# Kernel tuning notes

Measured on AMD Instinct MI355X. Metric: run time of the kernel, lower is better.

## Reference

```python
import jax, jax.numpy as jnp
import numpy as np

POOL = 7              # roi_size (output bins per side)
SAMPLING_RATIO = 2    # bilinear samples per bin side
POOLED_DIM = 5        # CEM_FILTER(245) // (7*7)
SPATIAL_SCALE = 0.0625  # 1/16 feature stride


def setup_inputs() -> dict:
    key = jax.random.key(0)
    k1, k2, k3 = jax.random.split(key, 3)
    B, C, H, W = 8, 245, 100, 100
    N = 512
    IMG = 1600.0
    x = jax.random.normal(k1, (B, C, H, W), dtype=jnp.float32)
    xy = jax.random.uniform(k2, (B, N, 2), minval=0.0, maxval=IMG - 256.0)
    wh = jax.random.uniform(k3, (B, N, 2), minval=16.0, maxval=256.0)
    boxes = jnp.concatenate([xy, xy + wh], axis=-1)  # (x1,y1,x2,y2) in image coords
    return {"x": x, "boxes": boxes}


def reference(x, boxes):
    """Position-sensitive RoIAlign (torchvision ps_roi_align semantics).
    x: [B, C=POOLED_DIM*POOL*POOL, H, W]; boxes: [B, N, 4] in image coords.
    Returns [B*N, POOLED_DIM, POOL, POOL]."""
    B, C, H, W = x.shape
    Bb, N, _ = boxes.shape
    R = Bb * N
    g, P, D, s = SAMPLING_RATIO, POOL, POOLED_DIM, SPATIAL_SCALE

    batch_idx = jnp.repeat(jnp.arange(Bb, dtype=jnp.int32), N)  # convert_to_roi_format ids
    rois = boxes.reshape(R, 4)

    # aligned roi coords on the feature map (half-pixel offset)
    start_w = rois[:, 0] * s - 0.5
    start_h = rois[:, 1] * s - 0.5
    end_w = rois[:, 2] * s - 0.5
    end_h = rois[:, 3] * s - 0.5
    bin_h = (end_h - start_h) / P
    bin_w = (end_w - start_w) / P

    p = jnp.arange(P, dtype=jnp.float32)
    i = jnp.arange(g, dtype=jnp.float32)
    # sample coordinates, shape [R, P, g]
    ys = start_h[:, None, None] + p[None, :, None] * bin_h[:, None, None] \
         + (i[None, None, :] + 0.5) * bin_h[:, None, None] / g
    xs = start_w[:, None, None] + p[None, :, None] * bin_w[:, None, None] \
         + (i[None, None, :] + 0.5) * bin_w[:, None, None] / g

    # zero outside [-1, H] / [-1, W] (torchvision bilinear_interpolate)
    vy = ((ys >= -1.0) & (ys <= H)).astype(x.dtype)  # [R,P,g]
    vx = ((xs >= -1.0) & (xs <= W)).astype(x.dtype)

    yc = jnp.clip(ys, 0.0, H - 1.0)
    xc = jnp.clip(xs, 0.0, W - 1.0)
    yl = jnp.floor(yc).astype(jnp.int32)
    xl = jnp.floor(xc).astype(jnp.int32)
    yh = jnp.minimum(yl + 1, H - 1)
    xh = jnp.minimum(xl + 1, W - 1)
    ly = yc - yl.astype(x.dtype); hy = 1.0 - ly
    lx = xc - xl.astype(x.dtype); hx = 1.0 - lx

    # position-sensitive input channel: c_in = (d*P + ph)*P + pw, shape [D,P,P]
    c_in = ((jnp.arange(D)[:, None, None] * P + jnp.arange(P)[None, :, None]) * P
            + jnp.arange(P)[None, None, :]).astype(jnp.int32)

    # broadcast to [R, D, P(h), P(w), g(h), g(w)]
    b = batch_idx[:, None, None, None, None, None]
    c = c_in[None, :, :, :, None, None]
    gy = lambda a: a[:, None, :, None, :, None]  # y-axis arrays [R,P,g]
    gx = lambda a: a[:, None, None, :, None, :]  # x-axis arrays [R,P,g]

    v11 = x[b, c, gy(yl), gx(xl)]
    v12 = x[b, c, gy(yl), gx(xh)]
    v21 = x[b, c, gy(yh), gx(xl)]
    v22 = x[b, c, gy(yh), gx(xh)]
    val = (gy(hy) * gx(hx) * v11 + gy(hy) * gx(lx) * v12
           + gy(ly) * gx(hx) * v21 + gy(ly) * gx(lx) * v22)
    val = val * (gy(vy) * gx(vx))
    out = val.sum(axis=(4, 5)) / (g * g)  # average over sampling grid -> [R, D, P, P]
    return out
```

## Files before the change

### kernel.cpp

```cpp
#include <hip/hip_runtime.h>

#define POOL 7
#define SCALE 0.0625f
#define HW 10000
#define NROI 512
#define NCH 245

typedef const __attribute__((address_space(1))) void* gas_ptr;
typedef __attribute__((address_space(3))) void* las_ptr;

__global__ __launch_bounds__(512) void psroi_kernel(
    const float* __restrict__ x, const float* __restrict__ boxes,
    float* __restrict__ ws, int H, int W)
{
    __shared__ float plane[HW + 4];

    int p = blockIdx.x;
    int b = p / NCH;
    int c = p - b * NCH;
    int ph = (c / POOL) % POOL;
    int pw = c % POOL;

    int n = threadIdx.x;
    int r = b * NROI + n;

    float4 bx = *(const float4*)(boxes + (size_t)r * 4);

    const float4* __restrict__ src4 = (const float4*)(x + (size_t)p * HW);
    int lane = threadIdx.x & 63;
    int wave = threadIdx.x >> 6;
    #pragma unroll
    for (int i = 0; i < 5; ++i) {
        int chunk_base = i * 512 + wave * 64;
        int chunk = chunk_base + lane;
        if (chunk < HW / 4) {
            __builtin_amdgcn_global_load_lds(
                (gas_ptr)(src4 + chunk),
                (las_ptr)((char*)plane + (size_t)chunk_base * 16),
                16, 0, 0);
        }
    }
    if (threadIdx.x < 4) plane[HW + threadIdx.x] = 0.f;

    float sw = bx.x * SCALE - 0.5f;
    float sh = bx.y * SCALE - 0.5f;
    float ew = bx.z * SCALE - 0.5f;
    float eh = bx.w * SCALE - 0.5f;
    float bin_h = (eh - sh) / (float)POOL;
    float bin_w = (ew - sw) / (float)POOL;
    float fy0 = sh + (float)ph * bin_h;
    float fx0 = sw + (float)pw * bin_w;

    int   rowa[2];
    int   rstep[2];
    float wyh[2], wyl[2];
    #pragma unroll
    for (int iy = 0; iy < 2; ++iy) {
        float y  = fy0 + ((float)iy + 0.5f) * bin_h * 0.5f;
        float vy = (y >= -1.0f && y <= (float)H) ? 1.0f : 0.0f;
        float yc = fminf(fmaxf(y, 0.0f), (float)(H - 1));
        int   yl = (int)floorf(yc);
        float ly = yc - (float)yl;
        wyl[iy] = ly * vy;
        wyh[iy] = (1.0f - ly) * vy;
        rowa[iy]  = yl * W;
        rstep[iy] = (yl < H - 1) ? W : 0;
    }
    int   colx[2];
    float wxh[2], wxl[2];
    #pragma unroll
    for (int ix = 0; ix < 2; ++ix) {
        float xf = fx0 + ((float)ix + 0.5f) * bin_w * 0.5f;
        float vx = (xf >= -1.0f && xf <= (float)W) ? 1.0f : 0.0f;
        float xc = fminf(fmaxf(xf, 0.0f), (float)(W - 1));
        int   xl = (int)floorf(xc);
        float lx = xc - (float)xl;
        wxl[ix] = lx * vx;
        wxh[ix] = (1.0f - lx) * vx;
        colx[ix] = xl;
    }

    __syncthreads();

    float sum = 0.f;
    #pragma unroll
    for (int iy = 0; iy < 2; ++iy) {
        #pragma unroll
        for (int ix = 0; ix < 2; ++ix) {
            int a0 = rowa[iy] + colx[ix];
            int a1 = a0 + rstep[iy];
            float v11 = plane[a0];
            float v12 = plane[a0 + 1];
            float v21 = plane[a1];
            float v22 = plane[a1 + 1];
            float top = wxh[ix] * v11 + wxl[ix] * v12;
            float bot = wxh[ix] * v21 + wxl[ix] * v22;
            sum = fmaf(wyh[iy], top, sum);
            sum = fmaf(wyl[iy], bot, sum);
        }
    }
    ws[(size_t)p * NROI + n] = sum * 0.25f;
}

#define TILE 32
__global__ __launch_bounds__(256) void transpose_kernel(
    const float* __restrict__ ws, float* __restrict__ out)
{
    __shared__ float tile[TILE][TILE + 1];
    int b  = blockIdx.z;
    int c0 = blockIdx.y * TILE;
    int n0 = blockIdx.x * TILE;
    const float* in = ws + (size_t)b * NCH * NROI;
    float* ob = out + (size_t)b * NROI * NCH;
    int tx = threadIdx.x;
    int ty = threadIdx.y;

    #pragma unroll
    for (int k = 0; k < 4; ++k) {
        int cc = c0 + ty + k * 8;
        if (cc < NCH) tile[ty + k * 8][tx] = in[(size_t)cc * NROI + n0 + tx];
    }
    __syncthreads();
    #pragma unroll
    for (int k = 0; k < 4; ++k) {
        int nn = n0 + ty + k * 8;
        int cc = c0 + tx;
        if (cc < NCH) ob[(size_t)nn * NCH + cc] = tile[tx][ty + k * 8];
    }
}

extern "C" void kernel_launch(void* const* d_in, const int* in_sizes, int n_in,
                              void* d_out, int out_size, void* d_ws, size_t ws_size,
                              hipStream_t stream) {
    const float* x     = (const float*)d_in[0];
    const float* boxes = (const float*)d_in[1];
    float* out = (float*)d_out;
    float* ws  = (float*)d_ws;

    const int H = 100, W = 100;
    (void)in_sizes; (void)n_in; (void)out_size; (void)ws_size;

    hipLaunchKernelGGL(psroi_kernel, dim3(8 * NCH), dim3(512), 0, stream,
                       x, boxes, ws, H, W);
    hipLaunchKernelGGL(transpose_kernel, dim3(NROI / TILE, (NCH + TILE - 1) / TILE, 8),
                       dim3(TILE, 8), 0, stream, ws, out);
}
```

Before: 22.07 us.

## Fuse transpose into psroi kernel with interleaved block-to-batch mapping

```diff
diff --git a/kernel.cpp b/kernel.cpp
--- a/kernel.cpp
+++ b/kernel.cpp
@@ -11,13 +11,14 @@
 
 __global__ __launch_bounds__(512) void psroi_kernel(
     const float* __restrict__ x, const float* __restrict__ boxes,
-    float* __restrict__ ws, int H, int W)
+    float* __restrict__ out, int H, int W)
 {
     __shared__ float plane[HW + 4];
 
-    int p = blockIdx.x;
-    int b = p / NCH;
-    int c = p - b * NCH;
+    int bid = blockIdx.x;
+    int b = bid & 7;
+    int c = bid >> 3;
+    int p = b * NCH + c;
     int ph = (c / POOL) % POOL;
     int pw = c % POOL;
 
@@ -51,8 +52,7 @@
     float fy0 = sh + (float)ph * bin_h;
     float fx0 = sw + (float)pw * bin_w;
 
-    int   rowa[2];
-    int   rstep[2];
+    int   rowa[2], rstep[2];
     float wyh[2], wyl[2];
     #pragma unroll
     for (int iy = 0; iy < 2; ++iy) {
@@ -99,34 +99,7 @@
             sum = fmaf(wyl[iy], bot, sum);
         }
     }
-    ws[(size_t)p * NROI + n] = sum * 0.25f;
-}
-
-#define TILE 32
-__global__ __launch_bounds__(256) void transpose_kernel(
-    const float* __restrict__ ws, float* __restrict__ out)
-{
-    __shared__ float tile[TILE][TILE + 1];
-    int b  = blockIdx.z;
-    int c0 = blockIdx.y * TILE;
-    int n0 = blockIdx.x * TILE;
-    const float* in = ws + (size_t)b * NCH * NROI;
-    float* ob = out + (size_t)b * NROI * NCH;
-    int tx = threadIdx.x;
-    int ty = threadIdx.y;
-
-    #pragma unroll
-    for (int k = 0; k < 4; ++k) {
-        int cc = c0 + ty + k * 8;
-        if (cc < NCH) tile[ty + k * 8][tx] = in[(size_t)cc * NROI + n0 + tx];
-    }
-    __syncthreads();
-    #pragma unroll
-    for (int k = 0; k < 4; ++k) {
-        int nn = n0 + ty + k * 8;
-        int cc = c0 + tx;
-        if (cc < NCH) ob[(size_t)nn * NCH + cc] = tile[tx][ty + k * 8];
-    }
+    out[(size_t)r * NCH + c] = sum * 0.25f;
 }
 
 extern "C" void kernel_launch(void* const* d_in, const int* in_sizes, int n_in,
@@ -135,13 +108,10 @@
     const float* x     = (const float*)d_in[0];
     const float* boxes = (const float*)d_in[1];
     float* out = (float*)d_out;
-    float* ws  = (float*)d_ws;
 
     const int H = 100, W = 100;
-    (void)in_sizes; (void)n_in; (void)out_size; (void)ws_size;
+    (void)in_sizes; (void)n_in; (void)out_size; (void)d_ws; (void)ws_size;
 
-    hipLaunchKernelGGL(psroi_kernel, dim3(8 * NCH), dim3(512), 0, stream,
-                       x, boxes, ws, H, W);
-    hipLaunchKernelGGL(transpose_kernel, dim3(NROI / TILE, (NCH + TILE - 1) / TILE, 8),
-                       dim3(TILE, 8), 0, stream, ws, out);
+    hipLaunchKernelGGL(psroi_kernel, dim3(NCH * 8), dim3(512), 0, stream,
+                       x, boxes, out, H, W);
 }
```

Result: faster. 19.20 us (-13.0%).
